# Kernel tuning notes

Hardware: AMD Instinct MI355X
Metric: run time of the kernel (lower is better)

The kernel has to match this reference:

```python
import jax, jax.numpy as jnp
import numpy as np

B, H, S, D = 2, 16, 2048, 64

def setup_inputs() -> dict:
    key = jax.random.key(0)
    kq, kk, kv = jax.random.split(key, 3)
    query = jax.random.normal(kq, (B, H, S, D), dtype=jnp.float32)
    key_t = jax.random.normal(kk, (B, H, S, D), dtype=jnp.float32)
    value = jax.random.normal(kv, (B, H, S, D), dtype=jnp.float32)
    return {"query": query, "key": key_t, "value": value}

def reference(query, key, value):
    d_k = query.shape[-1]
    scale = 1.0 / jnp.sqrt(jnp.asarray(d_k, dtype=query.dtype))
    # scores: [B, H, S, S]
    scores = jnp.einsum('bhqd,bhkd->bhqk', query, key) * scale
    p_attn = jax.nn.softmax(scores, axis=-1)
    output = jnp.einsum('bhqk,bhkd->bhqd', p_attn, value)
    return (output, p_attn)
```

## Files before the change

### kernel.cpp

```cpp
#include <hip/hip_runtime.h>

#define SS 2048
#define DD 64
#define QB 64
#define KVB 128
#define NT (SS / KVB)

typedef unsigned short ushort_t;
typedef __attribute__((ext_vector_type(4)))  float f32x4;
typedef __attribute__((ext_vector_type(16))) float f32x16;
typedef __attribute__((ext_vector_type(8)))  short bf16x8;
typedef __attribute__((ext_vector_type(2)))  unsigned int u32x2;

static __device__ __forceinline__ unsigned short f2bf(float f) {
    unsigned u = __builtin_bit_cast(unsigned, f);
    u += 0x7FFFu + ((u >> 16) & 1u);
    return (unsigned short)(u >> 16);
}

static __device__ __forceinline__ f32x16 zero16() {
    f32x16 z;
#pragma unroll
    for (int i = 0; i < 16; ++i) z[i] = 0.f;
    return z;
}

union PFrag { bf16x8 v; unsigned w[4]; };

#define GLL16(src, dst) \
    __builtin_amdgcn_global_load_lds((const __attribute__((address_space(1))) void*)(src), \
                                     (__attribute__((address_space(3))) void*)(dst), 16, 0, 0)

__global__ void prep(const float* __restrict__ K, const float* __restrict__ V,
                     ushort_t* __restrict__ Kbf, ushort_t* __restrict__ Vt)
{
    const int tid = threadIdx.x;
    if (blockIdx.x < 2048) {
        int i = blockIdx.x * 256 + tid;
        f32x4 a = ((const f32x4*)K)[2 * i];
        f32x4 b = ((const f32x4*)K)[2 * i + 1];
        bf16x8 o;
#pragma unroll
        for (int j = 0; j < 4; ++j) o[j] = (short)f2bf(a[j]);
#pragma unroll
        for (int j = 0; j < 4; ++j) o[4 + j] = (short)f2bf(b[j]);
        ((bf16x8*)Kbf)[i] = o;
        return;
    }
    __shared__ float tile[64][65];
    const int bid2 = blockIdx.x - 2048;
    const int hh = bid2 >> 5;
    const int kt = bid2 & 31;
#pragma unroll
    for (int it = 0; it < 4; ++it) {
        int m = it * 256 + tid;
        int r = m >> 4, c4 = m & 15;
        f32x4 v = *(const f32x4*)(V + ((size_t)(hh * SS + kt * 64 + r)) * DD + c4 * 4);
#pragma unroll
        for (int j = 0; j < 4; ++j) tile[r][c4 * 4 + j] = v[j];
    }
    __syncthreads();
#pragma unroll
    for (int it = 0; it < 2; ++it) {
        int m = it * 256 + tid;
        int d = m >> 3, c8 = m & 7;
        bf16x8 o;
#pragma unroll
        for (int j = 0; j < 8; ++j) o[j] = (short)f2bf(tile[c8 * 8 + j][d]);
        *(bf16x8*)(Vt + ((size_t)hh * DD + d) * SS + kt * 64 + c8 * 8) = o;
    }
}

__global__ __launch_bounds__(256, 2)
void attn_main9(const float* __restrict__ gQ, const ushort_t* __restrict__ Kbf,
                const ushort_t* __restrict__ Vtbf, float* __restrict__ gO,
                float* __restrict__ gP)
{
    __shared__ float lsm[4][32];
    __shared__ __attribute__((aligned(16))) char shraw[65536];
    ushort_t* stage = (ushort_t*)shraw;
    float*    osm   = (float*)shraw;

    const int tid  = threadIdx.x;
    const int lane = tid & 63;
    const int wave = tid >> 6;
    const int lo5  = lane & 31;
    const int hi   = lane >> 5;
    const int qs   = wave >> 1;
    const int sub  = wave & 1;

    const int bid  = blockIdx.x;
    const int wg   = (bid & 7) * 128 + (bid >> 3);
    const int head = wg >> 5;
    const int q0b  = (wg & 31) * QB;

    const float*    Qh = gQ   + (size_t)head * SS * DD;
    const ushort_t* Kh = Kbf  + (size_t)head * SS * DD;
    const ushort_t* Vh = Vtbf + (size_t)head * DD * SS;
    float* Oh = gO + (size_t)head * SS * DD;
    float* Ph = gP + (size_t)head * SS * SS;

    const float SCALE = 0.125f * 1.44269504088896340736f;

    const int qrow = q0b + qs * 32 + lo5;
    bf16x8 qf[4];
#pragma unroll
    for (int ks = 0; ks < 4; ++ks) {
        const float* qp = Qh + (size_t)qrow * DD + ks * 16 + hi * 8;
        f32x4 a = *(const f32x4*)(qp);
        f32x4 b = *(const f32x4*)(qp + 4);
        bf16x8 o;
#pragma unroll
        for (int j = 0; j < 4; ++j) o[j] = (short)f2bf(a[j] * SCALE);
#pragma unroll
        for (int j = 0; j < 4; ++j) o[4 + j] = (short)f2bf(b[j] * SCALE);
        qf[ks] = o;
    }

    const int lgrp = lane >> 3;
    const int kchk = (lane & 7) ^ lgrp;
    const ushort_t* srcK[4];
    const ushort_t* srcV[4];
#pragma unroll
    for (int j = 0; j < 4; ++j) {
        int W = wave * 4 + j;
        srcK[j] = Kh + (size_t)(W * 8 + lgrp) * DD + kchk * 8;
        int d = W * 4 + (lane >> 4);
        int vchk = (lane & 15) ^ (d & 7);
        srcV[j] = Vh + (size_t)d * SS + vchk * 8;
    }

#pragma unroll
    for (int j = 0; j < 4; ++j) GLL16(srcK[j], stage + (wave * 4 + j) * 512);
    __syncthreads();

    float ls0 = 0.f, ls1 = 0.f;
    for (int t = 0; t < NT; ++t) {
        const int buf = t & 1;
        if (t + 1 < NT) {
#pragma unroll
            for (int j = 0; j < 4; ++j)
                GLL16(srcK[j] + (size_t)(t + 1) * KVB * DD,
                      stage + (buf ^ 1) * 16384 + (wave * 4 + j) * 512);
        }
        const ushort_t* Ksb = stage + buf * 16384;
#pragma unroll
        for (int g64 = 0; g64 < 2; ++g64) {
            const int kvl = g64 * 64 + sub * 32 + lo5;
            f32x16 acc = zero16();
#pragma unroll
            for (int ks = 0; ks < 4; ++ks) {
                bf16x8 kf = *(const bf16x8*)(Ksb + kvl * 64 + ((((ks * 2) + hi) ^ (kvl & 7)) << 3));
                acc = __builtin_amdgcn_mfma_f32_32x32x16_bf16(kf, qf[ks], acc, 0, 0, 0);
            }
#pragma unroll
            for (int r = 0; r < 16; r += 2) {
                ls0 += __builtin_exp2f(acc[r]);
                ls1 += __builtin_exp2f(acc[r + 1]);
            }
        }
        __syncthreads();
    }
    float lsum = ls0 + ls1;
    lsum += __shfl_xor(lsum, 32);
    lsm[wave][lo5] = lsum;
    __syncthreads();
    const float rinv = 1.0f / (lsm[qs * 2][lo5] + lsm[qs * 2 + 1][lo5]);

    f32x16 o0 = zero16(), o1 = zero16();
    float* prow_base = Ph + (size_t)qrow * SS;

#pragma unroll
    for (int j = 0; j < 4; ++j) {
        GLL16(srcK[j], stage + (wave * 4 + j) * 512);
        GLL16(srcV[j], stage + 8192 + (wave * 4 + j) * 512);
    }
    __syncthreads();

    for (int t = 0; t < NT; ++t) {
        const int buf = t & 1;
        if (t + 1 < NT) {
#pragma unroll
            for (int j = 0; j < 4; ++j) {
                GLL16(srcK[j] + (size_t)(t + 1) * KVB * DD,
                      stage + (buf ^ 1) * 16384 + (wave * 4 + j) * 512);
                GLL16(srcV[j] + (size_t)(t + 1) * KVB,
                      stage + (buf ^ 1) * 16384 + 8192 + (wave * 4 + j) * 512);
            }
        }
        const ushort_t* Ksb = stage + buf * 16384;
        const ushort_t* Vtb = Ksb + 8192;

#pragma unroll
        for (int g64 = 0; g64 < 2; ++g64) {
            const int kvl = g64 * 64 + sub * 32 + lo5;
            f32x16 acc = zero16();
#pragma unroll
            for (int ks = 0; ks < 4; ++ks) {
                bf16x8 kf = *(const bf16x8*)(Ksb + kvl * 64 + ((((ks * 2) + hi) ^ (kvl & 7)) << 3));
                acc = __builtin_amdgcn_mfma_f32_32x32x16_bf16(kf, qf[ks], acc, 0, 0, 0);
            }
            float pr[16];
#pragma unroll
            for (int r = 0; r < 16; ++r) pr[r] = __builtin_exp2f(acc[r]);

            float* prow = prow_base + t * KVB + g64 * 64 + sub * 32;
#pragma unroll
            for (int g = 0; g < 4; ++g) {
                f32x4 st = { pr[4*g+0] * rinv, pr[4*g+1] * rinv, pr[4*g+2] * rinv, pr[4*g+3] * rinv };
                *(f32x4*)(prow + g * 8 + hi * 4) = st;
            }

            unsigned u[8];
#pragma unroll
            for (int j = 0; j < 8; ++j)
                u[j] = (unsigned)f2bf(pr[2*j]) | ((unsigned)f2bf(pr[2*j+1]) << 16);
            unsigned s0 = __shfl_xor(u[0], 32), s1 = __shfl_xor(u[1], 32);
            unsigned s2 = __shfl_xor(u[2], 32), s3 = __shfl_xor(u[3], 32);
            unsigned s4 = __shfl_xor(u[4], 32), s5 = __shfl_xor(u[5], 32);
            unsigned s6 = __shfl_xor(u[6], 32), s7 = __shfl_xor(u[7], 32);
            PFrag pf0, pf1;
            pf0.w[0] = hi ? s2 : u[0];  pf0.w[1] = hi ? s3 : u[1];
            pf0.w[2] = hi ? u[2] : s0;  pf0.w[3] = hi ? u[3] : s1;
            pf1.w[0] = hi ? s6 : u[4];  pf1.w[1] = hi ? s7 : u[5];
            pf1.w[2] = hi ? u[6] : s4;  pf1.w[3] = hi ? u[7] : s5;

#pragma unroll
            for (int dt = 0; dt < 2; ++dt) {
                int drow = dt * 32 + lo5;
                int c0 = (g64 << 3) + (((sub * 4) + 0 + hi) ^ (drow & 7));
                int c1 = (g64 << 3) + (((sub * 4) + 2 + hi) ^ (drow & 7));
                bf16x8 vf0 = *(const bf16x8*)(Vtb + drow * 128 + (c0 << 3));
                bf16x8 vf1 = *(const bf16x8*)(Vtb + drow * 128 + (c1 << 3));
                f32x16& od = dt ? o1 : o0;
                od = __builtin_amdgcn_mfma_f32_32x32x16_bf16(vf0, pf0.v, od, 0, 0, 0);
                od = __builtin_amdgcn_mfma_f32_32x32x16_bf16(vf1, pf1.v, od, 0, 0, 0);
            }
        }
        __syncthreads();
    }

#pragma unroll
    for (int dt = 0; dt < 2; ++dt) {
        const f32x16& od = dt ? o1 : o0;
#pragma unroll
        for (int g = 0; g < 4; ++g) {
#pragma unroll
            for (int j = 0; j < 4; ++j) {
                int d = dt * 32 + g * 8 + hi * 4 + j;
                osm[(wave * 64 + d) * 33 + lo5] = od[4 * g + j];
            }
        }
    }
    __syncthreads();
    {
        const int p  = tid >> 7;
        const int q  = (tid >> 2) & 31;
        const int d0 = (tid & 3) * 16;
        const float rq = 1.0f / (lsm[2 * p][q] + lsm[2 * p + 1][q]);
        float* op = Oh + (size_t)(q0b + p * 32 + q) * DD + d0;
#pragma unroll
        for (int v4 = 0; v4 < 4; ++v4) {
            f32x4 st;
#pragma unroll
            for (int j = 0; j < 4; ++j) {
                int d = d0 + v4 * 4 + j;
                st[j] = (osm[((2 * p) * 64 + d) * 33 + q] +
                         osm[((2 * p + 1) * 64 + d) * 33 + q]) * rq;
            }
            *(f32x4*)(op + v4 * 4) = st;
        }
    }
}

__global__ __launch_bounds__(256, 2)
void attn_fused(const float* __restrict__ gQ, const float* __restrict__ gK,
                const float* __restrict__ gV, float* __restrict__ gO,
                float* __restrict__ gP)
{
    __shared__ unsigned short Qs[128 * DD];
    __shared__ unsigned short Ks[64 * DD];
    __shared__ unsigned short Vt[DD * 64];

    const int tid  = threadIdx.x;
    const int lane = tid & 63;
    const int wave = tid >> 6;
    const int lo5  = lane & 31;
    const int hi   = lane >> 5;

    const int head = blockIdx.x >> 4;
    const int q0b  = (blockIdx.x & 15) * 128;

    const float* Qh = gQ + (size_t)head * SS * DD;
    const float* Kh = gK + (size_t)head * SS * DD;
    const float* Vh = gV + (size_t)head * SS * DD;
    float* Oh = gO + (size_t)head * SS * DD;
    float* Ph = gP + (size_t)head * SS * SS;

    const float SCALE = 0.125f * 1.44269504088896340736f;

#pragma unroll
    for (int it = 0; it < 8; ++it) {
        int m = it * 256 + tid;
        int q = m >> 4, d4 = m & 15;
        f32x4 v = *(const f32x4*)(Qh + (size_t)(q0b + q) * DD + d4 * 4);
        unsigned a = (unsigned)f2bf(v.x * SCALE) | ((unsigned)f2bf(v.y * SCALE) << 16);
        unsigned b = (unsigned)f2bf(v.z * SCALE) | ((unsigned)f2bf(v.w * SCALE) << 16);
        u32x2 w; w.x = a; w.y = b;
        *(u32x2*)(Qs + q * 64 + d4 * 4) = w;
    }
    __syncthreads();

    const int qrow = wave * 32 + lo5;
    bf16x8 qf[4];
#pragma unroll
    for (int ks = 0; ks < 4; ++ks)
        qf[ks] = *(const bf16x8*)(Qs + qrow * 64 + ks * 16 + hi * 8);

    auto stageK = [&](int kv0) {
#pragma unroll
        for (int it = 0; it < 4; ++it) {
            int m = it * 256 + tid;
            int kv = m >> 4, d4 = m & 15;
            f32x4 v = *(const f32x4*)(Kh + (size_t)(kv0 + kv) * DD + d4 * 4);
            unsigned a = (unsigned)f2bf(v.x) | ((unsigned)f2bf(v.y) << 16);
            unsigned b = (unsigned)f2bf(v.z) | ((unsigned)f2bf(v.w) << 16);
            int c16 = (d4 >> 1) ^ (kv & 7);
            u32x2 w; w.x = a; w.y = b;
            *(u32x2*)(Ks + kv * 64 + c16 * 8 + (d4 & 1) * 4) = w;
        }
    };
    auto stageV = [&](int kv0) {
#pragma unroll
        for (int it = 0; it < 2; ++it) {
            int m = it * 256 + tid;
            int kv2 = m >> 4, d4 = m & 15;
            const float* p0 = Vh + (size_t)(kv0 + kv2 * 2) * DD + d4 * 4;
            f32x4 v0 = *(const f32x4*)(p0);
            f32x4 v1 = *(const f32x4*)(p0 + DD);
#pragma unroll
            for (int c = 0; c < 4; ++c) {
                int d = d4 * 4 + c;
                unsigned u = (unsigned)f2bf(v0[c]) | ((unsigned)f2bf(v1[c]) << 16);
                int c16 = (kv2 >> 2) ^ (d & 7);
                *(unsigned*)(Vt + d * 64 + c16 * 8 + (kv2 & 3) * 2) = u;
            }
        }
    };

    float m_run = -1e30f, l_run = 0.f;
    for (int kv0 = 0; kv0 < SS; kv0 += 64) {
        __syncthreads();
        stageK(kv0);
        __syncthreads();
#pragma unroll
        for (int sub = 0; sub < 2; ++sub) {
            f32x16 acc = zero16();
            int kvl = sub * 32 + lo5;
#pragma unroll
            for (int ks = 0; ks < 4; ++ks) {
                bf16x8 kf = *(const bf16x8*)(Ks + kvl * 64 + ((((ks * 2) + hi) ^ (kvl & 7)) << 3));
                acc = __builtin_amdgcn_mfma_f32_32x32x16_bf16(kf, qf[ks], acc, 0, 0, 0);
            }
            float tm = acc[0];
#pragma unroll
            for (int r = 1; r < 16; ++r) tm = fmaxf(tm, acc[r]);
            float mn = fmaxf(m_run, tm);
            float sum = 0.f;
#pragma unroll
            for (int r = 0; r < 16; ++r) sum += __builtin_exp2f(acc[r] - mn);
            l_run = l_run * __builtin_exp2f(m_run - mn) + sum;
            m_run = mn;
        }
    }
    {
        float mo = __shfl_xor(m_run, 32);
        float mf = fmaxf(m_run, mo);
        float la = l_run * __builtin_exp2f(m_run - mf);
        float lb = __shfl_xor(la, 32);
        l_run = la + lb;
        m_run = mf;
    }
    const float rinv = 1.0f / l_run;

    f32x16 o0 = zero16(), o1 = zero16();
    const int qg = q0b + wave * 32 + lo5;
    float* prow_base = Ph + (size_t)qg * SS;

    for (int kv0 = 0; kv0 < SS; kv0 += 64) {
        __syncthreads();
        stageK(kv0);
        stageV(kv0);
        __syncthreads();
#pragma unroll
        for (int sub = 0; sub < 2; ++sub) {
            f32x16 acc = zero16();
            int kvl = sub * 32 + lo5;
#pragma unroll
            for (int ks = 0; ks < 4; ++ks) {
                bf16x8 kf = *(const bf16x8*)(Ks + kvl * 64 + ((((ks * 2) + hi) ^ (kvl & 7)) << 3));
                acc = __builtin_amdgcn_mfma_f32_32x32x16_bf16(kf, qf[ks], acc, 0, 0, 0);
            }
            float pr[16];
#pragma unroll
            for (int r = 0; r < 16; ++r) pr[r] = __builtin_exp2f(acc[r] - m_run);

            float* prow = prow_base + kv0 + sub * 32;
#pragma unroll
            for (int g = 0; g < 4; ++g) {
                f32x4 st = { pr[4*g+0] * rinv, pr[4*g+1] * rinv, pr[4*g+2] * rinv, pr[4*g+3] * rinv };
                *(f32x4*)(prow + g * 8 + hi * 4) = st;
            }

            unsigned u[8];
#pragma unroll
            for (int j = 0; j < 8; ++j)
                u[j] = (unsigned)f2bf(pr[2*j]) | ((unsigned)f2bf(pr[2*j+1]) << 16);

            unsigned s0 = __shfl_xor(u[0], 32), s1 = __shfl_xor(u[1], 32);
            unsigned s2 = __shfl_xor(u[2], 32), s3 = __shfl_xor(u[3], 32);
            unsigned s4 = __shfl_xor(u[4], 32), s5 = __shfl_xor(u[5], 32);
            unsigned s6 = __shfl_xor(u[6], 32), s7 = __shfl_xor(u[7], 32);
            PFrag pf0, pf1;
            pf0.w[0] = hi ? s2 : u[0];  pf0.w[1] = hi ? s3 : u[1];
            pf0.w[2] = hi ? u[2] : s0;  pf0.w[3] = hi ? u[3] : s1;
            pf1.w[0] = hi ? s6 : u[4];  pf1.w[1] = hi ? s7 : u[5];
            pf1.w[2] = hi ? u[6] : s4;  pf1.w[3] = hi ? u[7] : s5;

#pragma unroll
            for (int dt = 0; dt < 2; ++dt) {
                int drow = dt * 32 + lo5;
                int c0 = ((sub * 4) + 0 + hi) ^ (drow & 7);
                int c1 = ((sub * 4) + 2 + hi) ^ (drow & 7);
                bf16x8 vf0 = *(const bf16x8*)(Vt + drow * 64 + (c0 << 3));
                bf16x8 vf1 = *(const bf16x8*)(Vt + drow * 64 + (c1 << 3));
                f32x16& od = dt ? o1 : o0;
                od = __builtin_amdgcn_mfma_f32_32x32x16_bf16(vf0, pf0.v, od, 0, 0, 0);
                od = __builtin_amdgcn_mfma_f32_32x32x16_bf16(vf1, pf1.v, od, 0, 0, 0);
            }
        }
    }

    float* orow = Oh + (size_t)qg * DD;
#pragma unroll
    for (int dt = 0; dt < 2; ++dt) {
        const f32x16& od = dt ? o1 : o0;
#pragma unroll
        for (int g = 0; g < 4; ++g) {
            f32x4 st = { od[4*g+0] * rinv, od[4*g+1] * rinv, od[4*g+2] * rinv, od[4*g+3] * rinv };
            *(f32x4*)(orow + dt * 32 + g * 8 + hi * 4) = st;
        }
    }
}

extern "C" void kernel_launch(void* const* d_in, const int* in_sizes, int n_in,
                              void* d_out, int out_size, void* d_ws, size_t ws_size,
                              hipStream_t stream) {
    const float* Q = (const float*)d_in[0];
    const float* K = (const float*)d_in[1];
    const float* V = (const float*)d_in[2];
    float* O = (float*)d_out;
    float* P = O + (size_t)2 * 16 * SS * DD;

    const size_t HD = (size_t)32 * SS * DD;
    const size_t need = 2 * HD * sizeof(ushort_t);

    if (ws_size >= need) {
        ushort_t* Kbf  = (ushort_t*)d_ws;
        ushort_t* Vtbf = Kbf + HD;
        hipLaunchKernelGGL(prep, dim3(3072), dim3(256), 0, stream, K, V, Kbf, Vtbf);
        hipLaunchKernelGGL(attn_main9, dim3(1024), dim3(256), 0, stream, Q, Kbf, Vtbf, O, P);
    } else {
        hipLaunchKernelGGL(attn_fused, dim3(512), dim3(256), 0, stream, Q, K, V, O, P);
    }
}
```

Baseline: 216.9 us.

## Repartition waves so each covers all 64 queries over a 32-key slice

Each wave now holds Q fragments for both 32-row query halves and handles one 32-key slice of the 128-key tile, instead of one query half and two key slices. Each K fragment loaded from LDS now feeds two MFMAs, and each V fragment is reused across both query halves, which cuts LDS read traffic per MFMA. The cost is twice the accumulator and Q registers, which may hurt occupancy at two blocks per CU. Row sums and the output now need a four-way cross-wave reduction, done in two passes through shared memory with extra barriers.

Measured after the change: 228.0 us. +5.1%, slower.

```diff
diff --git a/kernel.cpp b/kernel.cpp
--- a/kernel.cpp
+++ b/kernel.cpp
@@ -72,11 +72,11 @@
 }
 
 __global__ __launch_bounds__(256, 2)
-void attn_main9(const float* __restrict__ gQ, const ushort_t* __restrict__ Kbf,
-                const ushort_t* __restrict__ Vtbf, float* __restrict__ gO,
-                float* __restrict__ gP)
+void attn_main10(const float* __restrict__ gQ, const ushort_t* __restrict__ Kbf,
+                 const ushort_t* __restrict__ Vtbf, float* __restrict__ gO,
+                 float* __restrict__ gP)
 {
-    __shared__ float lsm[4][32];
+    __shared__ float lsm[4][2][32];
     __shared__ __attribute__((aligned(16))) char shraw[65536];
     ushort_t* stage = (ushort_t*)shraw;
     float*    osm   = (float*)shraw;
@@ -86,8 +86,6 @@
     const int wave = tid >> 6;
     const int lo5  = lane & 31;
     const int hi   = lane >> 5;
-    const int qs   = wave >> 1;
-    const int sub  = wave & 1;
 
     const int bid  = blockIdx.x;
     const int wg   = (bid & 7) * 128 + (bid >> 3);
@@ -102,20 +100,21 @@
 
     const float SCALE = 0.125f * 1.44269504088896340736f;
 
-    const int qrow = q0b + qs * 32 + lo5;
-    bf16x8 qf[4];
-#pragma unroll
-    for (int ks = 0; ks < 4; ++ks) {
-        const float* qp = Qh + (size_t)qrow * DD + ks * 16 + hi * 8;
-        f32x4 a = *(const f32x4*)(qp);
-        f32x4 b = *(const f32x4*)(qp + 4);
-        bf16x8 o;
-#pragma unroll
-        for (int j = 0; j < 4; ++j) o[j] = (short)f2bf(a[j] * SCALE);
-#pragma unroll
-        for (int j = 0; j < 4; ++j) o[4 + j] = (short)f2bf(b[j] * SCALE);
-        qf[ks] = o;
-    }
+    bf16x8 qf2[2][4];
+#pragma unroll
+    for (int p = 0; p < 2; ++p)
+#pragma unroll
+        for (int ks = 0; ks < 4; ++ks) {
+            const float* qp = Qh + (size_t)(q0b + p * 32 + lo5) * DD + ks * 16 + hi * 8;
+            f32x4 a = *(const f32x4*)(qp);
+            f32x4 b = *(const f32x4*)(qp + 4);
+            bf16x8 o;
+#pragma unroll
+            for (int j = 0; j < 4; ++j) o[j] = (short)f2bf(a[j] * SCALE);
+#pragma unroll
+            for (int j = 0; j < 4; ++j) o[4 + j] = (short)f2bf(b[j] * SCALE);
+            qf2[p][ks] = o;
+        }
 
     const int lgrp = lane >> 3;
     const int kchk = (lane & 7) ^ lgrp;
@@ -129,12 +128,13 @@
         int vchk = (lane & 15) ^ (d & 7);
         srcV[j] = Vh + (size_t)d * SS + vchk * 8;
     }
+    const int kvl = wave * 32 + lo5;
 
 #pragma unroll
     for (int j = 0; j < 4; ++j) GLL16(srcK[j], stage + (wave * 4 + j) * 512);
     __syncthreads();
 
-    float ls0 = 0.f, ls1 = 0.f;
+    float ls00 = 0.f, ls01 = 0.f, ls10 = 0.f, ls11 = 0.f;
     for (int t = 0; t < NT; ++t) {
         const int buf = t & 1;
         if (t + 1 < NT) {
@@ -144,31 +144,37 @@
                       stage + (buf ^ 1) * 16384 + (wave * 4 + j) * 512);
         }
         const ushort_t* Ksb = stage + buf * 16384;
-#pragma unroll
-        for (int g64 = 0; g64 < 2; ++g64) {
-            const int kvl = g64 * 64 + sub * 32 + lo5;
-            f32x16 acc = zero16();
-#pragma unroll
-            for (int ks = 0; ks < 4; ++ks) {
-                bf16x8 kf = *(const bf16x8*)(Ksb + kvl * 64 + ((((ks * 2) + hi) ^ (kvl & 7)) << 3));
-                acc = __builtin_amdgcn_mfma_f32_32x32x16_bf16(kf, qf[ks], acc, 0, 0, 0);
-            }
-#pragma unroll
-            for (int r = 0; r < 16; r += 2) {
-                ls0 += __builtin_exp2f(acc[r]);
-                ls1 += __builtin_exp2f(acc[r + 1]);
-            }
-        }
-        __syncthreads();
-    }
-    float lsum = ls0 + ls1;
-    lsum += __shfl_xor(lsum, 32);
-    lsm[wave][lo5] = lsum;
+        bf16x8 kf[4];
+#pragma unroll
+        for (int ks = 0; ks < 4; ++ks)
+            kf[ks] = *(const bf16x8*)(Ksb + kvl * 64 + ((((ks * 2) + hi) ^ (kvl & 7)) << 3));
+        f32x16 a0 = zero16(), a1 = zero16();
+#pragma unroll
+        for (int ks = 0; ks < 4; ++ks) {
+            a0 = __builtin_amdgcn_mfma_f32_32x32x16_bf16(kf[ks], qf2[0][ks], a0, 0, 0, 0);
+            a1 = __builtin_amdgcn_mfma_f32_32x32x16_bf16(kf[ks], qf2[1][ks], a1, 0, 0, 0);
+        }
+#pragma unroll
+        for (int r = 0; r < 16; r += 2) {
+            ls00 += __builtin_exp2f(a0[r]);
+            ls01 += __builtin_exp2f(a0[r + 1]);
+            ls10 += __builtin_exp2f(a1[r]);
+            ls11 += __builtin_exp2f(a1[r + 1]);
+        }
+        __syncthreads();
+    }
+    {
+        float l0 = ls00 + ls01, l1 = ls10 + ls11;
+        l0 += __shfl_xor(l0, 32);
+        l1 += __shfl_xor(l1, 32);
+        lsm[wave][0][lo5] = l0;
+        lsm[wave][1][lo5] = l1;
+    }
     __syncthreads();
-    const float rinv = 1.0f / (lsm[qs * 2][lo5] + lsm[qs * 2 + 1][lo5]);
-
-    f32x16 o0 = zero16(), o1 = zero16();
-    float* prow_base = Ph + (size_t)qrow * SS;
+    const float rinv0 = 1.0f / (lsm[0][0][lo5] + lsm[1][0][lo5] + lsm[2][0][lo5] + lsm[3][0][lo5]);
+    const float rinv1 = 1.0f / (lsm[0][1][lo5] + lsm[1][1][lo5] + lsm[2][1][lo5] + lsm[3][1][lo5]);
+
+    f32x16 o00 = zero16(), o01 = zero16(), o10 = zero16(), o11 = zero16();
 
 #pragma unroll
     for (int j = 0; j < 4; ++j) {
@@ -191,20 +197,38 @@
         const ushort_t* Ksb = stage + buf * 16384;
         const ushort_t* Vtb = Ksb + 8192;
 
-#pragma unroll
-        for (int g64 = 0; g64 < 2; ++g64) {
-            const int kvl = g64 * 64 + sub * 32 + lo5;
-            f32x16 acc = zero16();
-#pragma unroll
-            for (int ks = 0; ks < 4; ++ks) {
-                bf16x8 kf = *(const bf16x8*)(Ksb + kvl * 64 + ((((ks * 2) + hi) ^ (kvl & 7)) << 3));
-                acc = __builtin_amdgcn_mfma_f32_32x32x16_bf16(kf, qf[ks], acc, 0, 0, 0);
-            }
+        bf16x8 kf[4];
+#pragma unroll
+        for (int ks = 0; ks < 4; ++ks)
+            kf[ks] = *(const bf16x8*)(Ksb + kvl * 64 + ((((ks * 2) + hi) ^ (kvl & 7)) << 3));
+        f32x16 a0 = zero16(), a1 = zero16();
+#pragma unroll
+        for (int ks = 0; ks < 4; ++ks) {
+            a0 = __builtin_amdgcn_mfma_f32_32x32x16_bf16(kf[ks], qf2[0][ks], a0, 0, 0, 0);
+            a1 = __builtin_amdgcn_mfma_f32_32x32x16_bf16(kf[ks], qf2[1][ks], a1, 0, 0, 0);
+        }
+
+        bf16x8 vf[2][2];
+#pragma unroll
+        for (int dt = 0; dt < 2; ++dt) {
+            int drow = dt * 32 + lo5;
+#pragma unroll
+            for (int ksub = 0; ksub < 2; ++ksub) {
+                int m = wave * 4 + ksub * 2 + hi;
+                int c = (m & 8) | ((m & 7) ^ (drow & 7));
+                vf[dt][ksub] = *(const bf16x8*)(Vtb + drow * 128 + (c << 3));
+            }
+        }
+
+#pragma unroll
+        for (int p = 0; p < 2; ++p) {
+            const f32x16& acc = p ? a1 : a0;
+            const float rinv = p ? rinv1 : rinv0;
             float pr[16];
 #pragma unroll
             for (int r = 0; r < 16; ++r) pr[r] = __builtin_exp2f(acc[r]);
 
-            float* prow = prow_base + t * KVB + g64 * 64 + sub * 32;
+            float* prow = Ph + (size_t)(q0b + p * 32 + lo5) * SS + t * KVB + wave * 32;
 #pragma unroll
             for (int g = 0; g < 4; ++g) {
                 f32x4 st = { pr[4*g+0] * rinv, pr[4*g+1] * rinv, pr[4*g+2] * rinv, pr[4*g+3] * rinv };
@@ -225,51 +249,49 @@
             pf1.w[0] = hi ? s6 : u[4];  pf1.w[1] = hi ? s7 : u[5];
             pf1.w[2] = hi ? u[6] : s4;  pf1.w[3] = hi ? u[7] : s5;
 
-#pragma unroll
-            for (int dt = 0; dt < 2; ++dt) {
-                int drow = dt * 32 + lo5;
-                int c0 = (g64 << 3) + (((sub * 4) + 0 + hi) ^ (drow & 7));
-                int c1 = (g64 << 3) + (((sub * 4) + 2 + hi) ^ (drow & 7));
-                bf16x8 vf0 = *(const bf16x8*)(Vtb + drow * 128 + (c0 << 3));
-                bf16x8 vf1 = *(const bf16x8*)(Vtb + drow * 128 + (c1 << 3));
-                f32x16& od = dt ? o1 : o0;
-                od = __builtin_amdgcn_mfma_f32_32x32x16_bf16(vf0, pf0.v, od, 0, 0, 0);
-                od = __builtin_amdgcn_mfma_f32_32x32x16_bf16(vf1, pf1.v, od, 0, 0, 0);
-            }
-        }
-        __syncthreads();
-    }
-
-#pragma unroll
-    for (int dt = 0; dt < 2; ++dt) {
-        const f32x16& od = dt ? o1 : o0;
-#pragma unroll
-        for (int g = 0; g < 4; ++g) {
-#pragma unroll
-            for (int j = 0; j < 4; ++j) {
-                int d = dt * 32 + g * 8 + hi * 4 + j;
-                osm[(wave * 64 + d) * 33 + lo5] = od[4 * g + j];
-            }
-        }
-    }
-    __syncthreads();
-    {
-        const int p  = tid >> 7;
-        const int q  = (tid >> 2) & 31;
-        const int d0 = (tid & 3) * 16;
-        const float rq = 1.0f / (lsm[2 * p][q] + lsm[2 * p + 1][q]);
-        float* op = Oh + (size_t)(q0b + p * 32 + q) * DD + d0;
-#pragma unroll
-        for (int v4 = 0; v4 < 4; ++v4) {
-            f32x4 st;
-#pragma unroll
-            for (int j = 0; j < 4; ++j) {
-                int d = d0 + v4 * 4 + j;
-                st[j] = (osm[((2 * p) * 64 + d) * 33 + q] +
-                         osm[((2 * p + 1) * 64 + d) * 33 + q]) * rq;
-            }
-            *(f32x4*)(op + v4 * 4) = st;
-        }
+            f32x16& od0 = p ? o10 : o00;
+            f32x16& od1 = p ? o11 : o01;
+            od0 = __builtin_amdgcn_mfma_f32_32x32x16_bf16(vf[0][0], pf0.v, od0, 0, 0, 0);
+            od0 = __builtin_amdgcn_mfma_f32_32x32x16_bf16(vf[0][1], pf1.v, od0, 0, 0, 0);
+            od1 = __builtin_amdgcn_mfma_f32_32x32x16_bf16(vf[1][0], pf0.v, od1, 0, 0, 0);
+            od1 = __builtin_amdgcn_mfma_f32_32x32x16_bf16(vf[1][1], pf1.v, od1, 0, 0, 0);
+        }
+        __syncthreads();
+    }
+
+#pragma unroll
+    for (int p = 0; p < 2; ++p) {
+#pragma unroll
+        for (int dt = 0; dt < 2; ++dt) {
+            const f32x16& od = p ? (dt ? o11 : o10) : (dt ? o01 : o00);
+#pragma unroll
+            for (int g = 0; g < 4; ++g) {
+#pragma unroll
+                for (int j = 0; j < 4; ++j) {
+                    int d = dt * 32 + g * 8 + hi * 4 + j;
+                    osm[(wave * 64 + d) * 33 + lo5] = od[4 * g + j];
+                }
+            }
+        }
+        __syncthreads();
+        {
+            const int q  = tid >> 3;
+            const int d0 = (tid & 7) * 8;
+            const float rq = 1.0f / (lsm[0][p][q] + lsm[1][p][q] + lsm[2][p][q] + lsm[3][p][q]);
+            float out[8];
+#pragma unroll
+            for (int i = 0; i < 8; ++i) {
+                int d = d0 + i;
+                out[i] = (osm[(0 * 64 + d) * 33 + q] + osm[(1 * 64 + d) * 33 + q] +
+                          osm[(2 * 64 + d) * 33 + q] + osm[(3 * 64 + d) * 33 + q]) * rq;
+            }
+            float* op = Oh + (size_t)(q0b + p * 32 + q) * DD + d0;
+            f32x4 x = { out[0], out[1], out[2], out[3] };
+            f32x4 y = { out[4], out[5], out[6], out[7] };
+            *(f32x4*)(op)     = x;
+            *(f32x4*)(op + 4) = y;
+        }
+        __syncthreads();
     }
 }
 
@@ -469,7 +491,7 @@
         ushort_t* Kbf  = (ushort_t*)d_ws;
         ushort_t* Vtbf = Kbf + HD;
         hipLaunchKernelGGL(prep, dim3(3072), dim3(256), 0, stream, K, V, Kbf, Vtbf);
-        hipLaunchKernelGGL(attn_main9, dim3(1024), dim3(256), 0, stream, Q, Kbf, Vtbf, O, P);
+        hipLaunchKernelGGL(attn_main10, dim3(1024), dim3(256), 0, stream, Q, Kbf, Vtbf, O, P);
     } else {
         hipLaunchKernelGGL(attn_fused, dim3(512), dim3(256), 0, stream, Q, K, V, O, P);
     }
```
